# Kernel optimization log

Measured on AMD Instinct MI355X. Metric: run time of the kernel, lower is better.

## Reference

```python
import jax, jax.numpy as jnp
import numpy as np

B, IN_DIM, K, D = 8192, 1024, 2048, 256
TAU = 1.0
BN_EPS = 1e-5


def setup_inputs() -> dict:
    key = jax.random.key(0)
    ks = jax.random.split(key, 4)
    x = jax.random.normal(ks[0], (B, IN_DIM), dtype=jnp.float32)
    u = jax.random.uniform(ks[1], (B, K), dtype=jnp.float32)  # uniform for gumbel noise
    W = jax.random.normal(ks[2], (IN_DIM, D), dtype=jnp.float32) * 0.02
    b = jnp.zeros((D,), dtype=jnp.float32)
    gamma = jnp.ones((D,), dtype=jnp.float32)
    beta = jnp.zeros((D,), dtype=jnp.float32)
    E = jax.random.normal(ks[3], (K, D), dtype=jnp.float32)  # nn.Embedding default N(0,1)
    return {"x": x, "u": u, "W": W, "b": b, "gamma": gamma, "beta": beta, "E": E}


def reference(x, u, W, b, gamma, beta, E):
    # classifier + BatchNorm1d (training mode: batch stats, biased variance)
    h = x @ W + b                                   # [B, D]
    mu = jnp.mean(h, axis=0)
    var = jnp.var(h, axis=0)
    h = (h - mu) * jax.lax.rsqrt(var + BN_EPS) * gamma + beta
    # negative squared euclidean distance via ||h||^2 - 2 h.E^T + ||e||^2 (GEMM form,
    # avoids materializing [B, K, D])
    h2 = jnp.sum(h * h, axis=-1, keepdims=True)     # [B, 1]
    e2 = jnp.sum(E * E, axis=-1)                    # [K]
    logits = -(h2 - 2.0 * (h @ E.T) + e2)           # [B, K]
    # gumbel-softmax (soft) with tau
    g = -jnp.log(-jnp.log(u + 1e-10) + 1e-10)
    assignments = jax.nn.softmax((logits + g) / TAU, axis=-1)  # [B, K]
    z = assignments @ E                             # [B, D]
    probs = jax.nn.softmax(logits, axis=-1)
    return probs, z
```

## Files before the change

kernel.cpp:

```cpp
#include <hip/hip_runtime.h>
#include <math.h>

#define B_SZ 8192
#define IN_DIM 1024
#define K_CB 2048
#define D_SZ 256
#define BN_EPS 1e-5f

typedef _Float16 f16;
typedef _Float16 f16x8 __attribute__((ext_vector_type(8)));
typedef _Float16 f16x4 __attribute__((ext_vector_type(4)));
typedef float    f32x4 __attribute__((ext_vector_type(4)));

#define GLOAD_LDS16(g, l) __builtin_amdgcn_global_load_lds(                      \
    (const __attribute__((address_space(1))) unsigned int*)(g),                  \
    (__attribute__((address_space(3))) unsigned int*)(l), 16, 0, 0)

template<int BM, int BN, int BK, int EPI, bool A32>
__global__ __launch_bounds__(256) void gemm_mfma(
    const void* __restrict__ Aptr, int lda,
    const f16* __restrict__ Bptr, int ldb,
    void* __restrict__ Cptr, int ldc, int Kdim,
    const float* __restrict__ bias)
{
    constexpr int G    = BK / 8;
    constexpr int MASK = G - 1;
    constexpr int WM = BM / 2, WN = BN / 2;
    constexpr int FM = WM / 16, FN = WN / 16;
    constexpr int CH_A = BM * G;
    constexpr int CH_B = BN * G;

    __shared__ char lds[(BM + BN) * BK * 2];
    char* As = lds;
    char* Bs = lds + BM * BK * 2;

    const int tid  = threadIdx.x;
    const int w    = tid >> 6, lane = tid & 63;
    const int wm   = w >> 1,   wn   = w & 1;
    const int row0 = blockIdx.x * BM;
    const int col0 = blockIdx.y * BN;

    f32x4 acc[FM][FN] = {};

    for (int k0 = 0; k0 < Kdim; k0 += BK) {
        #pragma unroll
        for (int i = 0; i < CH_B / 256; ++i) {
            const int base = (i * 4 + w) * 64;
            const int s = base + lane;
            const int r = s / G, c = s % G;
            const f16* src = Bptr + (size_t)(col0 + r) * ldb + k0 + ((c ^ (r & MASK)) * 8);
            GLOAD_LDS16(src, Bs + base * 16);
        }
        if (!A32) {
            #pragma unroll
            for (int i = 0; i < CH_A / 256; ++i) {
                const int base = (i * 4 + w) * 64;
                const int s = base + lane;
                const int r = s / G, c = s % G;
                const f16* src = (const f16*)Aptr + (size_t)(row0 + r) * lda + k0 + ((c ^ (r & MASK)) * 8);
                GLOAD_LDS16(src, As + base * 16);
            }
        } else {
            #pragma unroll
            for (int i = 0; i < CH_A / 256; ++i) {
                const int s = i * 256 + tid;
                const int r = s / G, c = s % G;
                const float* src = (const float*)Aptr + (size_t)(row0 + r) * lda + k0 + c * 8;
                const float4 v0 = ((const float4*)src)[0];
                const float4 v1 = ((const float4*)src)[1];
                f16x8 d;
                d[0] = (f16)v0.x; d[1] = (f16)v0.y; d[2] = (f16)v0.z; d[3] = (f16)v0.w;
                d[4] = (f16)v1.x; d[5] = (f16)v1.y; d[6] = (f16)v1.z; d[7] = (f16)v1.w;
                *(f16x8*)(As + (r * G + (c ^ (r & MASK))) * 16) = d;
            }
        }
        __syncthreads();

        #pragma unroll
        for (int kk = 0; kk < BK / 32; ++kk) {
            f16x8 af[FM], bf[FN];
            #pragma unroll
            for (int m = 0; m < FM; ++m) {
                const int r = wm * WM + m * 16 + (lane & 15);
                const int g = (kk * 4 + (lane >> 4)) ^ (r & MASK);
                af[m] = *(const f16x8*)(As + r * (BK * 2) + g * 16);
            }
            #pragma unroll
            for (int n = 0; n < FN; ++n) {
                const int r = wn * WN + n * 16 + (lane & 15);
                const int g = (kk * 4 + (lane >> 4)) ^ (r & MASK);
                bf[n] = *(const f16x8*)(Bs + r * (BK * 2) + g * 16);
            }
            #pragma unroll
            for (int m = 0; m < FM; ++m)
                #pragma unroll
                for (int n = 0; n < FN; ++n)
                    acc[m][n] = __builtin_amdgcn_mfma_f32_16x16x32_f16(af[m], bf[n], acc[m][n], 0, 0, 0);
        }
        __syncthreads();
    }

    #pragma unroll
    for (int m = 0; m < FM; ++m) {
        const int rbase = row0 + wm * WM + m * 16 + (lane >> 4) * 4;
        #pragma unroll
        for (int n = 0; n < FN; ++n) {
            const int c = col0 + wn * WN + n * 16 + (lane & 15);
            #pragma unroll
            for (int j = 0; j < 4; ++j) {
                const float v = acc[m][n][j];
                if (EPI == 0) {
                    ((float*)Cptr)[(size_t)(rbase + j) * ldc + c] = v;
                } else {
                    ((f16*)Cptr)[(size_t)(rbase + j) * ldc + c] = (f16)(v + bias[c]);
                }
            }
        }
    }
}

#define LVP 2052

__global__ __launch_bounds__(512, 2) void fused_sm(
    const f16* __restrict__ h16, const f16* __restrict__ E16,
    const float* __restrict__ e2v, const float* __restrict__ u,
    float* __restrict__ probs, f16* __restrict__ assign16)
{
    __shared__ __align__(16) char lds_raw[16 * LVP * 4];
    f16* Bs0 = (f16*)lds_raw;
    f16* Bs1 = Bs0 + 128 * 256;
    float* lv_lds = (float*)lds_raw;

    const int tid  = threadIdx.x;
    const int w    = tid >> 6, lane = tid & 63;
    const int q    = lane >> 4, r16 = lane & 15;
    const int row0 = blockIdx.x * 16;
    const int colL = w * 16 + r16;

    f16x8 af[8];
    {
        const f16* hrow = h16 + (size_t)(row0 + r16) * D_SZ + q * 8;
        #pragma unroll
        for (int kk = 0; kk < 8; ++kk) af[kk] = *(const f16x8*)(hrow + kk * 32);
    }

    f32x4 acc[16];
    #pragma unroll
    for (int n = 0; n < 16; ++n) acc[n] = (f32x4){0.f, 0.f, 0.f, 0.f};

    #pragma unroll
    for (int i = 0; i < 8; ++i) {
        const int base = (i * 8 + w) * 64;
        const int s = base + lane;
        const int r = s >> 5, cg = s & 31;
        GLOAD_LDS16(E16 + (size_t)r * D_SZ + ((cg ^ (r & 31)) * 8), Bs0 + base * 8);
    }

    #pragma unroll
    for (int c = 0; c < 16; ++c) {
        f16* buf = (c & 1) ? Bs1 : Bs0;
        f16* nbuf = (c & 1) ? Bs0 : Bs1;
        if (c < 15) {
            #pragma unroll
            for (int i = 0; i < 8; ++i) {
                const int base = (i * 8 + w) * 64;
                const int s = base + lane;
                const int r = s >> 5, cg = s & 31;
                GLOAD_LDS16(E16 + (size_t)((c + 1) * 128 + r) * D_SZ + ((cg ^ (r & 31)) * 8),
                            nbuf + base * 8);
            }
            asm volatile("s_waitcnt vmcnt(8)" ::: "memory");
        } else {
            asm volatile("s_waitcnt vmcnt(0)" ::: "memory");
        }
        __builtin_amdgcn_s_barrier();
        __builtin_amdgcn_sched_barrier(0);
        #pragma unroll
        for (int kk = 0; kk < 8; ++kk) {
            const int gb = (kk * 4 + q) ^ (colL & 31);
            const f16x8 bf = *(const f16x8*)(buf + colL * 256 + gb * 8);
            acc[c] = __builtin_amdgcn_mfma_f32_16x16x32_f16(af[kk], bf, acc[c], 0, 0, 0);
        }
        __builtin_amdgcn_sched_barrier(0);
        __builtin_amdgcn_s_barrier();
        __builtin_amdgcn_sched_barrier(0);
    }
    __syncthreads();

    #pragma unroll
    for (int n = 0; n < 16; ++n) {
        const float ec = e2v[n * 128 + colL];
        #pragma unroll
        for (int j = 0; j < 4; ++j) {
            lv_lds[(q * 4 + j) * LVP + n * 128 + colL] = 2.f * acc[n][j] - ec;
        }
    }
    __syncthreads();

    const int trow = tid >> 5;
    const int cg   = tid & 31;
    const float* urow = u + (size_t)(row0 + trow) * K_CB + cg * 4;
    const float* lrow = lv_lds + trow * LVP + cg * 4;

    float m1 = -1e30f, m2 = -1e30f;
    f16x4 gv[16];
    #pragma unroll
    for (int n = 0; n < 16; ++n) {
        const float4 u4 = *(const float4*)(urow + n * 128);
        const f32x4 l4 = *(const f32x4*)(lrow + n * 128);
        const float uu[4] = {u4.x, u4.y, u4.z, u4.w};
        #pragma unroll
        for (int e = 0; e < 4; ++e) {
            const float g = -__logf(-__logf(uu[e] + 1e-10f) + 1e-10f);
            gv[n][e] = (f16)g;
            m1 = fmaxf(m1, l4[e]);
            m2 = fmaxf(m2, l4[e] + (float)gv[n][e]);
        }
    }
    #pragma unroll
    for (int off = 1; off < 32; off <<= 1) {
        m1 = fmaxf(m1, __shfl_xor(m1, off));
        m2 = fmaxf(m2, __shfl_xor(m2, off));
    }

    float s1 = 0.f, s2 = 0.f;
    f32x4 p1[16];
    #pragma unroll
    for (int n = 0; n < 16; ++n) {
        const f32x4 l4 = *(const f32x4*)(lrow + n * 128);
        #pragma unroll
        for (int e = 0; e < 4; ++e) {
            const float a = __expf(l4[e] - m1);
            const float b = a * __expf((float)gv[n][e] + m1 - m2);
            p1[n][e] = a; gv[n][e] = (f16)b;
            s1 += a; s2 += b;
        }
    }
    #pragma unroll
    for (int off = 1; off < 32; off <<= 1) {
        s1 += __shfl_xor(s1, off);
        s2 += __shfl_xor(s2, off);
    }
    const float r1 = 1.f / s1;
    const float r2 = 1.f / s2;

    float* prow = probs + (size_t)(row0 + trow) * K_CB + cg * 4;
    f16* arow = assign16 + (size_t)(row0 + trow) * K_CB + cg * 4;
    #pragma unroll
    for (int n = 0; n < 16; ++n) {
        float4 o;
        o.x = p1[n][0] * r1; o.y = p1[n][1] * r1;
        o.z = p1[n][2] * r1; o.w = p1[n][3] * r1;
        *(float4*)(prow + n * 128) = o;
        f16x4 a4;
        #pragma unroll
        for (int e = 0; e < 4; ++e) a4[e] = (f16)((float)gv[n][e] * r2);
        *(f16x4*)(arow + n * 128) = a4;
    }
}

__global__ __launch_bounds__(256) void conv_WT(const float* __restrict__ W, f16* __restrict__ WT)
{
    const int r = blockIdx.x, c = threadIdx.x;
    WT[c * 1024 + r] = (f16)W[r * 256 + c];
}

__global__ __launch_bounds__(256) void conv_E2(const float* __restrict__ E,
                                               f16* __restrict__ E16, f16* __restrict__ ET,
                                               float* __restrict__ e2)
{
    const int r = blockIdx.x, c = threadIdx.x;
    const int wave = c >> 6, lane = c & 63;
    const float v = E[r * 256 + c];
    E16[r * 256 + c] = (f16)v;
    ET[c * 2048 + r] = (f16)v;
    float ss = v * v;
    #pragma unroll
    for (int off = 32; off > 0; off >>= 1) ss += __shfl_down(ss, off);
    __shared__ float s4[4];
    if (lane == 0) s4[wave] = ss;
    __syncthreads();
    if (c == 0) e2[r] = s4[0] + s4[1] + s4[2] + s4[3];
}

__global__ __launch_bounds__(256) void bn_partial(const f16* __restrict__ h16, float* __restrict__ part)
{
    const int d = threadIdx.x;
    const int blk = blockIdx.x;
    const int r0 = blk * (B_SZ / 128);
    float s = 0.f, sq = 0.f;
    for (int r = r0; r < r0 + (B_SZ / 128); ++r) {
        const float v = (float)h16[(size_t)r * D_SZ + d];
        s += v; sq += v * v;
    }
    part[blk * 512 + d]       = s;
    part[blk * 512 + 256 + d] = sq;
}

__global__ __launch_bounds__(256) void bn_finalize(
    const float* __restrict__ part, const float* __restrict__ gamma, const float* __restrict__ beta,
    float* __restrict__ scale, float* __restrict__ shift)
{
    const int d = threadIdx.x;
    float s = 0.f, sq = 0.f;
    for (int b = 0; b < 128; ++b) { s += part[b * 512 + d]; sq += part[b * 512 + 256 + d]; }
    const float mu  = s / (float)B_SZ;
    const float var = sq / (float)B_SZ - mu * mu;
    const float sc  = gamma[d] * rsqrtf(var + BN_EPS);
    scale[d] = sc;
    shift[d] = beta[d] - mu * sc;
}

__global__ __launch_bounds__(256) void norm_h(
    f16* __restrict__ h16, const float* __restrict__ scale, const float* __restrict__ shift)
{
    const int wave = threadIdx.x >> 6, lane = threadIdx.x & 63;
    const int row = blockIdx.x * 4 + wave;
    f16x4* hp = (f16x4*)(h16 + (size_t)row * D_SZ);
    f16x4 v = hp[lane];
    const float4 sc = ((const float4*)scale)[lane];
    const float4 sh = ((const float4*)shift)[lane];
    v[0] = (f16)fmaf((float)v[0], sc.x, sh.x);
    v[1] = (f16)fmaf((float)v[1], sc.y, sh.y);
    v[2] = (f16)fmaf((float)v[2], sc.z, sh.z);
    v[3] = (f16)fmaf((float)v[3], sc.w, sh.w);
    hp[lane] = v;
}

extern "C" void kernel_launch(void* const* d_in, const int* in_sizes, int n_in,
                              void* d_out, int out_size, void* d_ws, size_t ws_size,
                              hipStream_t stream)
{
    const float* x     = (const float*)d_in[0];
    const float* u     = (const float*)d_in[1];
    const float* W     = (const float*)d_in[2];
    const float* bias  = (const float*)d_in[3];
    const float* gamma = (const float*)d_in[4];
    const float* beta  = (const float*)d_in[5];
    const float* E     = (const float*)d_in[6];

    float* probs = (float*)d_out;
    float* z     = probs + (size_t)B_SZ * K_CB;

    char* ws = (char*)d_ws;
    f16* assign16 = (f16*)ws;  ws += (size_t)B_SZ * K_CB * 2;
    f16* h16 = (f16*)ws;       ws += (size_t)B_SZ * D_SZ * 2;
    f16* WT16 = (f16*)ws;      ws += (size_t)D_SZ * IN_DIM * 2;
    f16* E16 = (f16*)ws;       ws += (size_t)K_CB * D_SZ * 2;
    f16* ET16 = (f16*)ws;      ws += (size_t)D_SZ * K_CB * 2;
    float* part = (float*)ws;  ws += 128 * 512 * 4;
    float* scale = (float*)ws; ws += D_SZ * 4;
    float* shift = (float*)ws; ws += D_SZ * 4;
    float* e2 = (float*)ws;    ws += K_CB * 4;

    conv_WT<<<IN_DIM, 256, 0, stream>>>(W, WT16);
    conv_E2<<<K_CB, 256, 0, stream>>>(E, E16, ET16, e2);

    {
        dim3 g(B_SZ / 64, D_SZ / 64);
        gemm_mfma<64, 64, 64, 1, true><<<g, 256, 0, stream>>>(
            x, IN_DIM, WT16, IN_DIM, h16, D_SZ, IN_DIM, bias);
    }
    bn_partial<<<128, 256, 0, stream>>>(h16, part);
    bn_finalize<<<1, 256, 0, stream>>>(part, gamma, beta, scale, shift);
    norm_h<<<B_SZ / 4, 256, 0, stream>>>(h16, scale, shift);

    fused_sm<<<B_SZ / 16, 512, 0, stream>>>(h16, E16, e2, u, probs, assign16);

    {
        dim3 g(B_SZ / 64, D_SZ / 64);
        gemm_mfma<64, 64, 128, 0, false><<<g, 256, 0, stream>>>(
            assign16, K_CB, ET16, K_CB, z, D_SZ, K_CB, nullptr);
    }
}
```

Measured before the change: 124.9 us.

## Fuse BN normalization into fused_sm and overlap Gumbel noise with MFMA loop

```diff
diff --git a/kernel.cpp b/kernel.cpp
--- a/kernel.cpp
+++ b/kernel.cpp
@@ -124,6 +124,7 @@
 __global__ __launch_bounds__(512, 2) void fused_sm(
     const f16* __restrict__ h16, const f16* __restrict__ E16,
     const float* __restrict__ e2v, const float* __restrict__ u,
+    const float* __restrict__ scale, const float* __restrict__ shift,
     float* __restrict__ probs, f16* __restrict__ assign16)
 {
     __shared__ __align__(16) char lds_raw[16 * LVP * 4];
@@ -136,24 +137,48 @@
     const int q    = lane >> 4, r16 = lane & 15;
     const int row0 = blockIdx.x * 16;
     const int colL = w * 16 + r16;
+    const int trow = tid >> 5;
+    const int cg   = tid & 31;
+
+    const float* urow = u + (size_t)(row0 + trow) * K_CB + cg * 4;
+    float4 uu[16];
+    #pragma unroll
+    for (int n = 0; n < 16; ++n) uu[n] = *(const float4*)(urow + n * 128);
 
     f16x8 af[8];
     {
         const f16* hrow = h16 + (size_t)(row0 + r16) * D_SZ + q * 8;
         #pragma unroll
-        for (int kk = 0; kk < 8; ++kk) af[kk] = *(const f16x8*)(hrow + kk * 32);
+        for (int kk = 0; kk < 8; ++kk) {
+            const f16x8 raw = *(const f16x8*)(hrow + kk * 32);
+            const float4 scA = *(const float4*)(scale + kk * 32 + q * 8);
+            const float4 scB = *(const float4*)(scale + kk * 32 + q * 8 + 4);
+            const float4 shA = *(const float4*)(shift + kk * 32 + q * 8);
+            const float4 shB = *(const float4*)(shift + kk * 32 + q * 8 + 4);
+            f16x8 d;
+            d[0] = (f16)fmaf((float)raw[0], scA.x, shA.x);
+            d[1] = (f16)fmaf((float)raw[1], scA.y, shA.y);
+            d[2] = (f16)fmaf((float)raw[2], scA.z, shA.z);
+            d[3] = (f16)fmaf((float)raw[3], scA.w, shA.w);
+            d[4] = (f16)fmaf((float)raw[4], scB.x, shB.x);
+            d[5] = (f16)fmaf((float)raw[5], scB.y, shB.y);
+            d[6] = (f16)fmaf((float)raw[6], scB.z, shB.z);
+            d[7] = (f16)fmaf((float)raw[7], scB.w, shB.w);
+            af[kk] = d;
+        }
     }
 
     f32x4 acc[16];
     #pragma unroll
     for (int n = 0; n < 16; ++n) acc[n] = (f32x4){0.f, 0.f, 0.f, 0.f};
+    f16x4 gv[16];
 
     #pragma unroll
     for (int i = 0; i < 8; ++i) {
         const int base = (i * 8 + w) * 64;
         const int s = base + lane;
-        const int r = s >> 5, cg = s & 31;
-        GLOAD_LDS16(E16 + (size_t)r * D_SZ + ((cg ^ (r & 31)) * 8), Bs0 + base * 8);
+        const int r = s >> 5, cgg = s & 31;
+        GLOAD_LDS16(E16 + (size_t)r * D_SZ + ((cgg ^ (r & 31)) * 8), Bs0 + base * 8);
     }
 
     #pragma unroll
@@ -165,8 +190,8 @@
             for (int i = 0; i < 8; ++i) {
                 const int base = (i * 8 + w) * 64;
                 const int s = base + lane;
-                const int r = s >> 5, cg = s & 31;
-                GLOAD_LDS16(E16 + (size_t)((c + 1) * 128 + r) * D_SZ + ((cg ^ (r & 31)) * 8),
+                const int r = s >> 5, cgg = s & 31;
+                GLOAD_LDS16(E16 + (size_t)((c + 1) * 128 + r) * D_SZ + ((cgg ^ (r & 31)) * 8),
                             nbuf + base * 8);
             }
             asm volatile("s_waitcnt vmcnt(8)" ::: "memory");
@@ -184,6 +209,17 @@
         __builtin_amdgcn_sched_barrier(0);
         __builtin_amdgcn_s_barrier();
         __builtin_amdgcn_sched_barrier(0);
+        if (c >= 1 && c <= 4) {
+            const int b0 = (c - 1) * 4;
+            #pragma unroll
+            for (int nn = 0; nn < 4; ++nn) {
+                const float4 u4 = uu[b0 + nn];
+                const float ua[4] = {u4.x, u4.y, u4.z, u4.w};
+                #pragma unroll
+                for (int e = 0; e < 4; ++e)
+                    gv[b0 + nn][e] = (f16)(-__logf(-__logf(ua[e] + 1e-10f) + 1e-10f));
+            }
+        }
     }
     __syncthreads();
 
@@ -197,22 +233,14 @@
     }
     __syncthreads();
 
-    const int trow = tid >> 5;
-    const int cg   = tid & 31;
-    const float* urow = u + (size_t)(row0 + trow) * K_CB + cg * 4;
     const float* lrow = lv_lds + trow * LVP + cg * 4;
 
     float m1 = -1e30f, m2 = -1e30f;
-    f16x4 gv[16];
     #pragma unroll
     for (int n = 0; n < 16; ++n) {
-        const float4 u4 = *(const float4*)(urow + n * 128);
         const f32x4 l4 = *(const f32x4*)(lrow + n * 128);
-        const float uu[4] = {u4.x, u4.y, u4.z, u4.w};
         #pragma unroll
         for (int e = 0; e < 4; ++e) {
-            const float g = -__logf(-__logf(uu[e] + 1e-10f) + 1e-10f);
-            gv[n][e] = (f16)g;
             m1 = fmaxf(m1, l4[e]);
             m2 = fmaxf(m2, l4[e] + (float)gv[n][e]);
         }
@@ -309,22 +337,6 @@
     const float sc  = gamma[d] * rsqrtf(var + BN_EPS);
     scale[d] = sc;
     shift[d] = beta[d] - mu * sc;
-}
-
-__global__ __launch_bounds__(256) void norm_h(
-    f16* __restrict__ h16, const float* __restrict__ scale, const float* __restrict__ shift)
-{
-    const int wave = threadIdx.x >> 6, lane = threadIdx.x & 63;
-    const int row = blockIdx.x * 4 + wave;
-    f16x4* hp = (f16x4*)(h16 + (size_t)row * D_SZ);
-    f16x4 v = hp[lane];
-    const float4 sc = ((const float4*)scale)[lane];
-    const float4 sh = ((const float4*)shift)[lane];
-    v[0] = (f16)fmaf((float)v[0], sc.x, sh.x);
-    v[1] = (f16)fmaf((float)v[1], sc.y, sh.y);
-    v[2] = (f16)fmaf((float)v[2], sc.z, sh.z);
-    v[3] = (f16)fmaf((float)v[3], sc.w, sh.w);
-    hp[lane] = v;
 }
 
 extern "C" void kernel_launch(void* const* d_in, const int* in_sizes, int n_in,
@@ -363,9 +375,8 @@
     }
     bn_partial<<<128, 256, 0, stream>>>(h16, part);
     bn_finalize<<<1, 256, 0, stream>>>(part, gamma, beta, scale, shift);
-    norm_h<<<B_SZ / 4, 256, 0, stream>>>(h16, scale, shift);
-
-    fused_sm<<<B_SZ / 16, 512, 0, stream>>>(h16, E16, e2, u, probs, assign16);
+
+    fused_sm<<<B_SZ / 16, 512, 0, stream>>>(h16, E16, e2, u, scale, shift, probs, assign16);
 
     {
         dim3 g(B_SZ / 64, D_SZ / 64);
```

Result: no change. 126.2 us (+1.0%).
